# Kernel optimization log

Measured on AMD Instinct MI355X. Metric: run time of the kernel, lower is better.

## Reference

```python
import jax, jax.numpy as jnp
import numpy as np

B, L = 64, 262144
KERNEL_SIZES = [65, 33, 17, 9]
K_LIST = [L // ks for ks in KERNEL_SIZES]  # sparsity_density per kernel


def conv1d_same(x, w):
    # x: [B, 1, L], w: [kernel_size] -> torch F.conv1d(..., padding='same')
    return jax.lax.conv_general_dilated(
        x, w[None, None, :], window_strides=(1,), padding='SAME',
        dimension_numbers=('NCH', 'OIH', 'NCH'))


def topk_absolutes_1d(x, k):
    # keep the k largest-|x| entries along the last axis, zero elsewhere
    _, idx = jax.lax.top_k(jnp.abs(x), k)          # [B, 1, k]
    kept = jnp.take_along_axis(x, idx, axis=-1)    # [B, 1, k]
    b = jnp.arange(x.shape[0])[:, None, None]
    c = jnp.arange(x.shape[1])[None, :, None]
    return jnp.zeros_like(x).at[b, c, idx].set(kept)


def setup_inputs() -> dict:
    key = jax.random.key(0)
    batch_x = jax.random.normal(key, (B, 1, L), dtype=jnp.float32)
    inp = {'batch_x': batch_x}
    for i, ks in enumerate(KERNEL_SIZES):
        inp[f'w{i}'] = 0.1 * jnp.ones((ks,), dtype=jnp.float32)
    return inp


def reference(batch_x, w0, w1, w2, w3):
    weights = [w0, w1, w2, w3]
    recon_sum = jnp.zeros_like(batch_x)
    for w, k in zip(weights, K_LIST):
        similarity = conv1d_same(batch_x, w)
        activations = topk_absolutes_1d(similarity, k)
        recon_sum = recon_sum + conv1d_same(activations, w)
    return recon_sum
```

## Files before the change

kernel.cpp:

```cpp
#include <hip/hip_runtime.h>
#include <stdint.h>


#define B_ 64
#define L_ 262144
#define NBINS 8192
#define CAPC 8192
#define LCAP 1024
#define TSUB 2304
#define SUBS 8
#define NCHUNK 15
#define T5 2304
#define NT5 114
#define NSCAN 16

typedef unsigned int u32;

__device__ const int d_K[4] = {4032, 7943, 15420, 29127};

template<int KS>
__device__ __forceinline__ void k1_body(
    const float* __restrict__ xr, const float* __restrict__ w,
    float* __restrict__ yrow, u32* __restrict__ gh,
    float* xbuf, u32* h32)
{
  constexpr int PAD = KS / 2;
  constexpr int OFF = 32 - PAD;
  const int tid = threadIdx.x;

  float wreg[KS];
#pragma unroll
  for (int j = 0; j < KS; ++j) wreg[j] = w[j];

  for (int i = tid; i < NBINS / 2; i += 256) h32[i] = 0u;
  __syncthreads();

  for (int it = 0; it < SUBS; ++it) {
    const int base = (blockIdx.x * SUBS + it) * TSUB;
    if (base >= L_) break;
    const bool interior = (base >= 32) && (base + TSUB + 32 <= L_);
    if (interior) {
      const float4* src = (const float4*)(xr + base - 32);
      for (int i = tid; i < (TSUB + 64) / 4; i += 256)
        ((float4*)xbuf)[i] = src[i];
    } else {
      for (int i = tid; i < TSUB + 64; i += 256) {
        int g = base - 32 + i;
        xbuf[i] = (g >= 0 && g < L_) ? xr[g] : 0.0f;
      }
    }
    __syncthreads();

    float acc[9];
#pragma unroll
    for (int r = 0; r < 9; ++r) acc[r] = 0.0f;
    const int q0 = tid * 9;
#pragma unroll
    for (int p = 0; p < KS + 8; ++p) {
      float xv = xbuf[q0 + OFF + p];
#pragma unroll
      for (int r = 0; r < 9; ++r) {
        const int j = p - r;
        if (j >= 0 && j < KS) acc[r] = fmaf(xv, wreg[j], acc[r]);
      }
    }
#pragma unroll
    for (int r = 0; r < 9; ++r) {
      int g = base + q0 + r;
      if (g < L_) {
        u32 ab = __float_as_uint(acc[r]) & 0x7fffffffu;
        u32 bin = ab >> 18;
        atomicAdd(&h32[bin >> 1], 1u << (16 * (bin & 1)));
      }
    }
    __syncthreads();
#pragma unroll
    for (int r = 0; r < 9; ++r) xbuf[q0 + r] = acc[r];
    __syncthreads();
    const int n4 = (min(TSUB, L_ - base)) / 4;
    float4* dst = (float4*)(yrow + base);
    for (int i = tid; i < n4; i += 256) dst[i] = ((const float4*)xbuf)[i];
    __syncthreads();
  }

  for (int i = tid; i < NBINS / 2; i += 256) {
    u32 v = h32[i];
    u32 lo = v & 0xffffu, hi = v >> 16;
    if (lo) atomicAdd(&gh[2 * i], lo);
    if (hi) atomicAdd(&gh[2 * i + 1], hi);
  }
}

__global__ __launch_bounds__(256) void k1_hist(
    const float* __restrict__ x, const float* __restrict__ w0,
    const float* __restrict__ w1, const float* __restrict__ w2,
    const float* __restrict__ w3, float* __restrict__ y,
    u32* __restrict__ ghist, int kk0, int ng)
{
  __shared__ __align__(16) float xbuf[TSUB + 64];
  __shared__ u32 h32[NBINS / 2];
  const int kg = blockIdx.y;
  const int row = blockIdx.z;
  const int rkl = row * ng + kg;
  const int kk = kk0 + kg;
  const float* xr = x + (size_t)row * L_;
  float* yrow = y + (size_t)rkl * L_;
  u32* gh = ghist + (size_t)rkl * NBINS;
  switch (kk) {
    case 0:  k1_body<65>(xr, w0, yrow, gh, xbuf, h32); break;
    case 1:  k1_body<33>(xr, w1, yrow, gh, xbuf, h32); break;
    case 2:  k1_body<17>(xr, w2, yrow, gh, xbuf, h32); break;
    default: k1_body< 9>(xr, w3, yrow, gh, xbuf, h32); break;
  }
}

__global__ __launch_bounds__(256) void k2_findbin(
    const u32* __restrict__ ghist, u32* __restrict__ bbin, u32* __restrict__ rrem,
    int kk0, int ng)
{
  __shared__ u32 h[NBINS];
  __shared__ u32 ssum[256];
  const int rkl = blockIdx.x;
  const u32 k = (u32)d_K[kk0 + (rkl % ng)];
  const u32* gh = ghist + (size_t)rkl * NBINS;
  for (int i = threadIdx.x; i < NBINS; i += 256) h[i] = gh[i];
  __syncthreads();
  u32 s = 0;
  for (int i = 0; i < 32; ++i) s += h[threadIdx.x * 32 + i];
  ssum[threadIdx.x] = s;
  __syncthreads();
  if (threadIdx.x == 0) {
    u32 cum = 0; int b = 0;
    for (int t = 255; t >= 0; --t) {
      if (cum + ssum[t] >= k) {
        for (int i = t * 32 + 31; i >= t * 32; --i) {
          if (cum + h[i] >= k) { b = i; break; }
          cum += h[i];
        }
        break;
      }
      cum += ssum[t];
    }
    bbin[rkl] = (u32)b;
    rrem[rkl] = k - cum;
  }
}

__global__ __launch_bounds__(256) void k3_scan(
    const float* __restrict__ y, const u32* __restrict__ bbin,
    u32* __restrict__ ccount, uint2* __restrict__ cand, int ng)
{
  __shared__ uint2 lcand[LCAP];
  __shared__ u32 lmeta[3];
  const int tid = threadIdx.x;
  const int rkl = blockIdx.z * ng + blockIdx.y;
  const u32 target = bbin[rkl];
  if (tid == 0) lmeta[0] = 0u;
  __syncthreads();
  const float* yr = y + (size_t)rkl * L_;
  const int c0 = blockIdx.x * (L_ / NSCAN);
  const float4* src = (const float4*)(yr + c0);
  for (int i = tid; i < (L_ / NSCAN) / 4; i += 256) {
    float4 v = src[i];
    const float* vf = (const float*)&v;
#pragma unroll
    for (int c = 0; c < 4; ++c) {
      u32 ab = __float_as_uint(vf[c]) & 0x7fffffffu;
      if ((ab >> 18) == target) {
        u32 slot = atomicAdd(&lmeta[0], 1u);
        if (slot < LCAP) lcand[slot] = make_uint2(ab, (u32)(c0 + 4 * i + c));
      }
    }
  }
  __syncthreads();
  if (tid == 0) {
    u32 m = lmeta[0]; if (m > LCAP) m = LCAP;
    lmeta[1] = m;
    lmeta[2] = atomicAdd(&ccount[rkl], m);
  }
  __syncthreads();
  const u32 m = lmeta[1], bse = lmeta[2];
  uint2* cd = cand + (size_t)rkl * CAPC;
  for (u32 i = tid; i < m; i += 256)
    if (bse + i < CAPC) cd[bse + i] = lcand[i];
}

__global__ __launch_bounds__(256) void k4_select(
    const uint2* __restrict__ cand, const u32* __restrict__ ccount,
    const u32* __restrict__ bbinA, const u32* __restrict__ rremA,
    u32* __restrict__ thr, u32* __restrict__ keepAll,
    u32* __restrict__ excN, u32* __restrict__ excL)
{
  __shared__ u32 cab[CAPC];
  __shared__ u32 h64[64];
  __shared__ u32 sh[3];
  __shared__ u32 lidx[64];
  __shared__ u32 lcnt;
  const int rkl = blockIdx.x;
  int n = (int)min(ccount[rkl], (u32)CAPC);
  u32 r = rremA[rkl];
  if (r > (u32)n) r = (u32)n;
  const uint2* cd = cand + (size_t)rkl * CAPC;
  for (int i = threadIdx.x; i < n; i += 256) cab[i] = cd[i].x & 0x3ffffu;

  u32 sel = 0;
  for (int round = 0; round < 3; ++round) {
    const int shift = 12 - 6 * round;
    const u32 himask = (round == 0) ? 0u : ((0x3ffffu << (shift + 6)) & 0x3ffffu);
    if (threadIdx.x < 64) h64[threadIdx.x] = 0u;
    __syncthreads();
    for (int i = threadIdx.x; i < n; i += 256) {
      u32 v = cab[i];
      if ((v & himask) == (sel & himask)) atomicAdd(&h64[(v >> shift) & 63u], 1u);
    }
    __syncthreads();
    if (threadIdx.x == 0) {
      u32 cum = 0; int d = 0;
      for (int dd = 63; dd >= 0; --dd) {
        if (cum + h64[dd] >= r) { d = dd; break; }
        cum += h64[dd];
      }
      sh[0] = (u32)d;
      sh[1] = r - cum;
      sh[2] = h64[d];
    }
    __syncthreads();
    sel |= sh[0] << shift;
    r = sh[1];
  }
  const u32 dup = sh[2];
  const u32 m = r;
  if (threadIdx.x == 0) thr[rkl] = (bbinA[rkl] << 18) | sel;

  if (m >= dup) {
    if (threadIdx.x == 0) { keepAll[rkl] = 1u; excN[rkl] = 0u; }
    return;
  }
  if (threadIdx.x == 0) lcnt = 0u;
  __syncthreads();
  for (int i = threadIdx.x; i < n; i += 256) {
    if (cab[i] == sel) {
      u32 s2 = atomicAdd(&lcnt, 1u);
      if (s2 < 64) lidx[s2] = cd[i].y;
    }
  }
  __syncthreads();
  if (threadIdx.x == 0) {
    int c = (int)min(lcnt, 64u);
    for (int i = 1; i < c; ++i) {
      u32 v = lidx[i]; int j = i - 1;
      while (j >= 0 && lidx[j] > v) { lidx[j + 1] = lidx[j]; --j; }
      lidx[j + 1] = v;
    }
    u32 mm = min(m, 32u);
    keepAll[rkl] = 0u; excN[rkl] = mm;
    for (u32 i = 0; i < mm; ++i) excL[(size_t)rkl * 32 + i] = lidx[i];
  }
}

__device__ __forceinline__ float k5_mask(float yv, int g, u32 t_ab, u32 ka,
                                         u32 en, const u32* __restrict__ excp)
{
  u32 ab = __float_as_uint(yv) & 0x7fffffffu;
  bool keep = ab > t_ab;
  if (ab == t_ab) {
    if (ka) keep = true;
    else {
      for (u32 e = 0; e < en; ++e)
        if (excp[e] == (u32)g) { keep = true; break; }
    }
  }
  return keep ? yv : 0.0f;
}

template<int KS>
__device__ __forceinline__ void k5_conv(
    const float* __restrict__ w, const float* abuf, float* accO)
{
  constexpr int PAD = KS / 2;
  constexpr int OFF2 = 32 - PAD;
  float wreg[KS];
#pragma unroll
  for (int j = 0; j < KS; ++j) wreg[j] = w[j];
  const int o0 = threadIdx.x * 9;
#pragma unroll
  for (int p = 0; p < KS + 8; ++p) {
    float av = abuf[o0 + OFF2 + p];
#pragma unroll
    for (int r = 0; r < 9; ++r) {
      const int j = p - r;
      if (j >= 0 && j < KS) accO[r] = fmaf(av, wreg[j], accO[r]);
    }
  }
}

__global__ __launch_bounds__(256) void k5_final(
    const float* __restrict__ y, const float* __restrict__ w0,
    const float* __restrict__ w1, const float* __restrict__ w2,
    const float* __restrict__ w3, const u32* __restrict__ thr,
    const u32* __restrict__ keepAll, const u32* __restrict__ excN,
    const u32* __restrict__ excL, float* __restrict__ out,
    int kk0, int ng)
{
  __shared__ __align__(16) float abuf[T5 + 64];
  const int tid = threadIdx.x;
  const int row = blockIdx.y;
  const int tile0 = blockIdx.x * T5;
  float accO[9];
#pragma unroll
  for (int r = 0; r < 9; ++r) accO[r] = 0.0f;

  for (int kg = 0; kg < ng; ++kg) {
    const int rkl = row * ng + kg;
    const int kk = kk0 + kg;
    const u32 t_ab = thr[rkl], ka = keepAll[rkl], en = excN[rkl];
    const u32* excp = excL + (size_t)rkl * 32;
    const float* yr = y + (size_t)rkl * L_;
    const bool interior = (tile0 >= 32) && (tile0 + T5 + 32 <= L_);
    if (interior) {
      const float4* src = (const float4*)(yr + tile0 - 32);
      for (int i = tid; i < (T5 + 64) / 4; i += 256) {
        float4 v = src[i];
        float* vf = (float*)&v;
#pragma unroll
        for (int c = 0; c < 4; ++c)
          vf[c] = k5_mask(vf[c], tile0 - 32 + 4 * i + c, t_ab, ka, en, excp);
        ((float4*)abuf)[i] = v;
      }
    } else {
      for (int i = tid; i < T5 + 64; i += 256) {
        int g = tile0 - 32 + i;
        float av = 0.0f;
        if (g >= 0 && g < L_) av = k5_mask(yr[g], g, t_ab, ka, en, excp);
        abuf[i] = av;
      }
    }
    __syncthreads();
    switch (kk) {
      case 0:  k5_conv<65>(w0, abuf, accO); break;
      case 1:  k5_conv<33>(w1, abuf, accO); break;
      case 2:  k5_conv<17>(w2, abuf, accO); break;
      default: k5_conv< 9>(w3, abuf, accO); break;
    }
    __syncthreads();
  }

  const int o0 = tid * 9;
#pragma unroll
  for (int r = 0; r < 9; ++r) abuf[o0 + r] = accO[r];
  __syncthreads();
  float* orow = out + (size_t)row * L_ + tile0;
  const int n4 = (min(T5, L_ - tile0)) / 4;
  if (kk0 == 0) {
    for (int i = tid; i < n4; i += 256)
      ((float4*)orow)[i] = ((const float4*)abuf)[i];
  } else {
    for (int i = tid; i < n4; i += 256) {
      float4 prev = ((const float4*)orow)[i];
      float4 add = ((const float4*)abuf)[i];
      prev.x += add.x; prev.y += add.y; prev.z += add.z; prev.w += add.w;
      ((float4*)orow)[i] = prev;
    }
  }
}

extern "C" void kernel_launch(void* const* d_in, const int* in_sizes, int n_in,
                              void* d_out, int out_size, void* d_ws, size_t ws_size,
                              hipStream_t stream)
{
  (void)in_sizes; (void)n_in; (void)out_size;
  const float* x  = (const float*)d_in[0];
  const float* w0 = (const float*)d_in[1];
  const float* w1 = (const float*)d_in[2];
  const float* w2 = (const float*)d_in[3];
  const float* w3 = (const float*)d_in[4];
  float* out = (float*)d_out;

  auto need = [](int ng) -> size_t {
    return (size_t)ng * 64 * ((size_t)L_ * 4 + NBINS * 4 + 4 * 6 + 32 * 4 + CAPC * 8);
  };
  int ng = 1;
  if (ws_size >= need(4)) ng = 4;
  else if (ws_size >= need(2)) ng = 2;

  const size_t NRK = (size_t)64 * ng;
  float* y     = (float*)d_ws;
  u32* ghist   = (u32*)(y + NRK * L_);
  u32* ccount  = ghist + NRK * NBINS;
  u32* bbin    = ccount + NRK;
  u32* rrem    = bbin + NRK;
  u32* thr     = rrem + NRK;
  u32* kAll    = thr + NRK;
  u32* excN    = kAll + NRK;
  u32* excL    = excN + NRK;
  uint2* cand  = (uint2*)(excL + NRK * 32);

  for (int kk0 = 0; kk0 < 4; kk0 += ng) {
    hipMemsetAsync(ghist, 0, (NRK * NBINS + NRK) * sizeof(u32), stream);
    dim3 g1(NCHUNK, ng, B_);
    k1_hist<<<g1, 256, 0, stream>>>(x, w0, w1, w2, w3, y, ghist, kk0, ng);
    k2_findbin<<<(int)NRK, 256, 0, stream>>>(ghist, bbin, rrem, kk0, ng);
    dim3 g3(NSCAN, ng, B_);
    k3_scan<<<g3, 256, 0, stream>>>(y, bbin, ccount, cand, ng);
    k4_select<<<(int)NRK, 256, 0, stream>>>(cand, ccount, bbin, rrem, thr, kAll, excN, excL);
    dim3 g5(NT5, B_);
    k5_final<<<g5, 256, 0, stream>>>(y, w0, w1, w2, w3, thr, kAll, excN, excL, out, kk0, ng);
  }
}
```

Before: 526.0 us.

## Double-buffer conv input via direct-to-LDS loads, fuse findbin into scan, direct stores

The histogram/conv kernel now stages input tiles with global_load_lds into two LDS buffers, prefetching the next tile while computing the current one. Results are written straight from registers to global memory instead of bouncing through LDS with extra barriers. The find-bin kernel is merged into the scan kernel, so each scan block recomputes the threshold bin from the histogram and one launch is removed. The final kernel also stores its outputs directly from registers. The trade-offs are strided, less coalesced 9-float-per-thread global stores, redundant histogram reads in every scan block, and the prefetch having no explicit wait on the async LDS loads beyond the existing barrier.

Result: faster. 502.8 us (-4.4%).

```diff
diff --git a/kernel.cpp b/kernel.cpp
--- a/kernel.cpp
+++ b/kernel.cpp
@@ -10,6 +10,7 @@
 #define TSUB 2304
 #define SUBS 8
 #define NCHUNK 15
+#define XSTG 2560
 #define T5 2304
 #define NT5 114
 #define NSCAN 16
@@ -17,12 +18,37 @@
 typedef unsigned int u32;
 
 __device__ const int d_K[4] = {4032, 7943, 15420, 29127};
+
+__device__ __forceinline__ void k1_stage(const float* __restrict__ xr, int base,
+                                         float* dst, int tid)
+{
+  const bool interior = (base >= 32) && (base - 32 + XSTG <= L_);
+  if (interior) {
+    const float* g0 = xr + (base - 32);
+    const int wv = tid >> 6, lane = tid & 63;
+#pragma unroll
+    for (int r = 0; r < 3; ++r) {
+      const int off = (r * 4 + wv) * 256;
+      if (off < XSTG) {
+        __builtin_amdgcn_global_load_lds(
+            (const __attribute__((address_space(1))) unsigned int*)(const void*)(g0 + off + lane * 4),
+            (__attribute__((address_space(3))) unsigned int*)(void*)(dst + off),
+            16, 0, 0);
+      }
+    }
+  } else {
+    for (int i = tid; i < TSUB + 64; i += 256) {
+      const int g = base - 32 + i;
+      dst[i] = (g >= 0 && g < L_) ? xr[g] : 0.0f;
+    }
+  }
+}
 
 template<int KS>
 __device__ __forceinline__ void k1_body(
     const float* __restrict__ xr, const float* __restrict__ w,
     float* __restrict__ yrow, u32* __restrict__ gh,
-    float* xbuf, u32* h32)
+    float* xb0, float* xb1, u32* h32)
 {
   constexpr int PAD = KS / 2;
   constexpr int OFF = 32 - PAD;
@@ -33,23 +59,19 @@
   for (int j = 0; j < KS; ++j) wreg[j] = w[j];
 
   for (int i = tid; i < NBINS / 2; i += 256) h32[i] = 0u;
+
+  const int base0 = blockIdx.x * SUBS * TSUB;
+  k1_stage(xr, base0, xb0, tid);
   __syncthreads();
 
   for (int it = 0; it < SUBS; ++it) {
-    const int base = (blockIdx.x * SUBS + it) * TSUB;
+    const int base = base0 + it * TSUB;
     if (base >= L_) break;
-    const bool interior = (base >= 32) && (base + TSUB + 32 <= L_);
-    if (interior) {
-      const float4* src = (const float4*)(xr + base - 32);
-      for (int i = tid; i < (TSUB + 64) / 4; i += 256)
-        ((float4*)xbuf)[i] = src[i];
-    } else {
-      for (int i = tid; i < TSUB + 64; i += 256) {
-        int g = base - 32 + i;
-        xbuf[i] = (g >= 0 && g < L_) ? xr[g] : 0.0f;
-      }
-    }
-    __syncthreads();
+    float* cur = (it & 1) ? xb1 : xb0;
+    float* nxt = (it & 1) ? xb0 : xb1;
+    const int nbase = base + TSUB;
+    if (it + 1 < SUBS && nbase < L_)
+      k1_stage(xr, nbase, nxt, tid);
 
     float acc[9];
 #pragma unroll
@@ -57,29 +79,33 @@
     const int q0 = tid * 9;
 #pragma unroll
     for (int p = 0; p < KS + 8; ++p) {
-      float xv = xbuf[q0 + OFF + p];
+      float xv = cur[q0 + OFF + p];
 #pragma unroll
       for (int r = 0; r < 9; ++r) {
         const int j = p - r;
         if (j >= 0 && j < KS) acc[r] = fmaf(xv, wreg[j], acc[r]);
       }
     }
+
+    const int g0 = base + q0;
+    if (g0 + 9 <= L_) {
+      float* yp = yrow + g0;
+#pragma unroll
+      for (int r = 0; r < 9; ++r) yp[r] = acc[r];
+    } else {
+#pragma unroll
+      for (int r = 0; r < 9; ++r)
+        if (g0 + r < L_) yrow[g0 + r] = acc[r];
+    }
+
 #pragma unroll
     for (int r = 0; r < 9; ++r) {
-      int g = base + q0 + r;
-      if (g < L_) {
+      if (g0 + r < L_) {
         u32 ab = __float_as_uint(acc[r]) & 0x7fffffffu;
         u32 bin = ab >> 18;
         atomicAdd(&h32[bin >> 1], 1u << (16 * (bin & 1)));
       }
     }
-    __syncthreads();
-#pragma unroll
-    for (int r = 0; r < 9; ++r) xbuf[q0 + r] = acc[r];
-    __syncthreads();
-    const int n4 = (min(TSUB, L_ - base)) / 4;
-    float4* dst = (float4*)(yrow + base);
-    for (int i = tid; i < n4; i += 256) dst[i] = ((const float4*)xbuf)[i];
     __syncthreads();
   }
 
@@ -97,7 +123,7 @@
     const float* __restrict__ w3, float* __restrict__ y,
     u32* __restrict__ ghist, int kk0, int ng)
 {
-  __shared__ __align__(16) float xbuf[TSUB + 64];
+  __shared__ __align__(16) float xb[2][XSTG];
   __shared__ u32 h32[NBINS / 2];
   const int kg = blockIdx.y;
   const int row = blockIdx.z;
@@ -107,29 +133,34 @@
   float* yrow = y + (size_t)rkl * L_;
   u32* gh = ghist + (size_t)rkl * NBINS;
   switch (kk) {
-    case 0:  k1_body<65>(xr, w0, yrow, gh, xbuf, h32); break;
-    case 1:  k1_body<33>(xr, w1, yrow, gh, xbuf, h32); break;
-    case 2:  k1_body<17>(xr, w2, yrow, gh, xbuf, h32); break;
-    default: k1_body< 9>(xr, w3, yrow, gh, xbuf, h32); break;
-  }
-}
-
-__global__ __launch_bounds__(256) void k2_findbin(
-    const u32* __restrict__ ghist, u32* __restrict__ bbin, u32* __restrict__ rrem,
-    int kk0, int ng)
+    case 0:  k1_body<65>(xr, w0, yrow, gh, xb[0], xb[1], h32); break;
+    case 1:  k1_body<33>(xr, w1, yrow, gh, xb[0], xb[1], h32); break;
+    case 2:  k1_body<17>(xr, w2, yrow, gh, xb[0], xb[1], h32); break;
+    default: k1_body< 9>(xr, w3, yrow, gh, xb[0], xb[1], h32); break;
+  }
+}
+
+__global__ __launch_bounds__(256) void k3_scan(
+    const float* __restrict__ y, const u32* __restrict__ ghist,
+    u32* __restrict__ bbin, u32* __restrict__ rrem,
+    u32* __restrict__ ccount, uint2* __restrict__ cand, int kk0, int ng)
 {
   __shared__ u32 h[NBINS];
   __shared__ u32 ssum[256];
-  const int rkl = blockIdx.x;
-  const u32 k = (u32)d_K[kk0 + (rkl % ng)];
+  __shared__ uint2 lcand[LCAP];
+  __shared__ u32 lmeta[5];
+  const int tid = threadIdx.x;
+  const int rkl = blockIdx.z * ng + blockIdx.y;
+  const u32 k = (u32)d_K[kk0 + blockIdx.y];
   const u32* gh = ghist + (size_t)rkl * NBINS;
-  for (int i = threadIdx.x; i < NBINS; i += 256) h[i] = gh[i];
+  for (int i = tid; i < NBINS; i += 256) h[i] = gh[i];
+  if (tid == 0) lmeta[0] = 0u;
   __syncthreads();
   u32 s = 0;
-  for (int i = 0; i < 32; ++i) s += h[threadIdx.x * 32 + i];
-  ssum[threadIdx.x] = s;
-  __syncthreads();
-  if (threadIdx.x == 0) {
+  for (int i = 0; i < 32; ++i) s += h[tid * 32 + i];
+  ssum[tid] = s;
+  __syncthreads();
+  if (tid == 0) {
     u32 cum = 0; int b = 0;
     for (int t = 255; t >= 0; --t) {
       if (cum + ssum[t] >= k) {
@@ -141,22 +172,12 @@
       }
       cum += ssum[t];
     }
-    bbin[rkl] = (u32)b;
-    rrem[rkl] = k - cum;
-  }
-}
-
-__global__ __launch_bounds__(256) void k3_scan(
-    const float* __restrict__ y, const u32* __restrict__ bbin,
-    u32* __restrict__ ccount, uint2* __restrict__ cand, int ng)
-{
-  __shared__ uint2 lcand[LCAP];
-  __shared__ u32 lmeta[3];
-  const int tid = threadIdx.x;
-  const int rkl = blockIdx.z * ng + blockIdx.y;
-  const u32 target = bbin[rkl];
-  if (tid == 0) lmeta[0] = 0u;
-  __syncthreads();
+    lmeta[3] = (u32)b;
+    if (blockIdx.x == 0) { bbin[rkl] = (u32)b; rrem[rkl] = k - cum; }
+  }
+  __syncthreads();
+  const u32 target = lmeta[3];
+
   const float* yr = y + (size_t)rkl * L_;
   const int c0 = blockIdx.x * (L_ / NSCAN);
   const float4* src = (const float4*)(yr + c0);
@@ -345,21 +366,27 @@
     __syncthreads();
   }
 
-  const int o0 = tid * 9;
-#pragma unroll
-  for (int r = 0; r < 9; ++r) abuf[o0 + r] = accO[r];
-  __syncthreads();
-  float* orow = out + (size_t)row * L_ + tile0;
-  const int n4 = (min(T5, L_ - tile0)) / 4;
+  const int g0 = tile0 + tid * 9;
+  float* orow = out + (size_t)row * L_;
   if (kk0 == 0) {
-    for (int i = tid; i < n4; i += 256)
-      ((float4*)orow)[i] = ((const float4*)abuf)[i];
+    if (g0 + 9 <= L_) {
+      float* op = orow + g0;
+#pragma unroll
+      for (int r = 0; r < 9; ++r) op[r] = accO[r];
+    } else {
+#pragma unroll
+      for (int r = 0; r < 9; ++r)
+        if (g0 + r < L_) orow[g0 + r] = accO[r];
+    }
   } else {
-    for (int i = tid; i < n4; i += 256) {
-      float4 prev = ((const float4*)orow)[i];
-      float4 add = ((const float4*)abuf)[i];
-      prev.x += add.x; prev.y += add.y; prev.z += add.z; prev.w += add.w;
-      ((float4*)orow)[i] = prev;
+    if (g0 + 9 <= L_) {
+      float* op = orow + g0;
+#pragma unroll
+      for (int r = 0; r < 9; ++r) op[r] += accO[r];
+    } else {
+#pragma unroll
+      for (int r = 0; r < 9; ++r)
+        if (g0 + r < L_) orow[g0 + r] += accO[r];
     }
   }
 }
@@ -399,9 +426,8 @@
     hipMemsetAsync(ghist, 0, (NRK * NBINS + NRK) * sizeof(u32), stream);
     dim3 g1(NCHUNK, ng, B_);
     k1_hist<<<g1, 256, 0, stream>>>(x, w0, w1, w2, w3, y, ghist, kk0, ng);
-    k2_findbin<<<(int)NRK, 256, 0, stream>>>(ghist, bbin, rrem, kk0, ng);
     dim3 g3(NSCAN, ng, B_);
-    k3_scan<<<g3, 256, 0, stream>>>(y, bbin, ccount, cand, ng);
+    k3_scan<<<g3, 256, 0, stream>>>(y, ghist, bbin, rrem, ccount, cand, kk0, ng);
     k4_select<<<(int)NRK, 256, 0, stream>>>(cand, ccount, bbin, rrem, thr, kAll, excN, excL);
     dim3 g5(NT5, B_);
     k5_final<<<g5, 256, 0, stream>>>(y, w0, w1, w2, w3, thr, kAll, excN, excL, out, kk0, ng);
```
